# Kernel tuning notes

Hardware: AMD Instinct MI355X
Metric: run time of the kernel (lower is better)

## Reference

```python
import jax, jax.numpy as jnp
import numpy as np

K = 1024          # num_embeddings
D = 64            # embedding_dim
COMMIT = 0.25
DIVERSITY = 0.1


def setup_inputs() -> dict:
    key = jax.random.key(0)
    k1, k2 = jax.random.split(key)
    inputs = jax.random.normal(k1, (64, D, 32, 32), dtype=jnp.float32)
    emb = jax.random.uniform(k2, (K, D), dtype=jnp.float32,
                             minval=-1.0 / K, maxval=1.0 / K)
    return {"inputs": inputs, "emb": emb}


def reference(inputs, emb):
    # NCHW -> NHWC, flatten to [N, D]
    x = jnp.transpose(inputs, (0, 2, 3, 1))          # [B,H,W,D]
    flat = x.reshape(-1, D)                           # [N,D]

    dist = (jnp.sum(flat * flat, axis=1, keepdims=True)
            + jnp.sum(emb * emb, axis=1)
            - 2.0 * flat @ emb.T)
    idx = jnp.argmin(dist, axis=1)                    # [N]
    encodings = jax.nn.one_hot(idx, K, dtype=flat.dtype)  # [N,K]

    # codebook lookup (equivalent to encodings @ emb)
    quantized = jnp.take(emb, idx, axis=0).reshape(x.shape)  # [B,H,W,D]

    sg = jax.lax.stop_gradient
    e_latent_loss = jnp.mean((sg(quantized) - x) ** 2)
    q_latent_loss = jnp.mean((quantized - sg(x)) ** 2)

    avg_probs = jnp.mean(encodings, axis=0)           # [K]
    perplexity = jnp.exp(-jnp.sum(avg_probs * jnp.log(avg_probs + 1e-10)))
    diversity_loss = DIVERSITY * (K - perplexity) / K

    loss = q_latent_loss + COMMIT * e_latent_loss + diversity_loss

    # straight-through estimator
    quantized_st = x + sg(quantized - x)
    quant_out = jnp.transpose(quantized_st, (0, 3, 1, 2))  # NHWC -> NCHW

    return loss, quant_out, perplexity, encodings, idx[:, None]
```

## Files before the change

### kernel.cpp

```cpp
#include <hip/hip_runtime.h>
#include <math.h>

namespace {
constexpr int Kc = 1024;
constexpr int Dd = 64;

__device__ inline float np_sumsq64(const float* __restrict__ a) {
#pragma clang fp contract(off)
    float r[8];
    #pragma unroll
    for (int j = 0; j < 8; ++j) r[j] = a[j] * a[j];
    #pragma unroll
    for (int i = 8; i < 64; i += 8) {
        #pragma unroll
        for (int j = 0; j < 8; ++j) {
            float s = a[i + j] * a[i + j];
            r[j] = r[j] + s;
        }
    }
    return ((r[0] + r[1]) + (r[2] + r[3])) + ((r[4] + r[5]) + (r[6] + r[7]));
}

__global__ void k_ee(const float* __restrict__ emb, float* __restrict__ ee) {
    int k = blockIdx.x * blockDim.x + threadIdx.x;
    ee[k] = np_sumsq64(emb + (size_t)k * Dd);
}

__global__ __launch_bounds__(256, 4) void k_main(
    const float* __restrict__ inputs, const float* __restrict__ emb,
    const float* __restrict__ ee_g, float* __restrict__ quant,
    float* __restrict__ enc, float* __restrict__ idx_out,
    unsigned int* __restrict__ hist, float* __restrict__ partials)
{
    __shared__ float sb[4][64];
    __shared__ int   si[4][64];

    const int tid = threadIdx.x;
    const int p = __builtin_amdgcn_readfirstlane(tid >> 6);
    const int l = tid & 63;
    const int n = blockIdx.x * 64 + l;
    const int b = n >> 10;
    const int hw = n & 1023;

    const float* xin = inputs + (size_t)b * (Dd * 1024) + hw;
    float x[Dd];
    #pragma unroll
    for (int d = 0; d < Dd; ++d) x[d] = xin[d * 1024];

    const float xx = np_sumsq64(x);

    float4* enc4 = (float4*)enc + (size_t)blockIdx.x * 16384 + tid;

    float best = INFINITY;
    int i1 = 0;
    const int k0 = p * 256;
    for (int kk = 0; kk < 256; ++kk) {
        const int k = __builtin_amdgcn_readfirstlane(k0 + kk);
        const float* ek = emb + (size_t)k * Dd;
        float g = 0.f;
        #pragma unroll
        for (int d = 0; d < Dd; ++d) g = fmaf(x[d], ek[d], g);
        float A = xx + ee_g[k];
        float dist = fmaf(-2.f, g, A);
        bool lt = dist < best;
        best = lt ? dist : best;
        i1   = lt ? k    : i1;
        if ((kk & 3) == 0) {
            *enc4 = float4{0.f, 0.f, 0.f, 0.f};
            enc4 += 256;
        }
    }

    sb[p][l] = best; si[p][l] = i1;
    __syncthreads();

    if (tid < 64) {
        best = INFINITY; i1 = 0;
        #pragma unroll
        for (int q = 0; q < 4; ++q) {
            float s = sb[q][l];
            int   i = si[q][l];
            bool lt = s < best;
            best = lt ? s : best;
            i1   = lt ? i : i1;
        }

        {
            const float4* eb = (const float4*)(emb + (size_t)i1 * Dd);
            float* qout = quant + (size_t)b * (Dd * 1024) + hw;
            #pragma unroll
            for (int i = 0; i < Dd / 4; ++i) {
                float4 v = eb[i];
                qout[(i * 4 + 0) * 1024] = v.x;
                qout[(i * 4 + 1) * 1024] = v.y;
                qout[(i * 4 + 2) * 1024] = v.z;
                qout[(i * 4 + 3) * 1024] = v.w;
            }
        }

        idx_out[n] = (float)i1;
        atomicAdd(hist + i1, 1u);

        enc[(size_t)n * Kc + i1] = 1.0f;

        float v = best;
        #pragma unroll
        for (int off = 32; off > 0; off >>= 1) v += __shfl_down(v, off, 64);
        if (l == 0) partials[blockIdx.x] = v;
    }
}

__global__ __launch_bounds__(1024) void k_fin(
    const unsigned int* __restrict__ hist, const float* __restrict__ partials,
    float* __restrict__ loss_out, float* __restrict__ perp_out)
{
    __shared__ double sd[1024];
    int tid = threadIdx.x;
    double p = (double)hist[tid] * (1.0 / 65536.0);
    sd[tid] = p * log(p + 1e-10);
    __syncthreads();
    for (int s = 512; s > 0; s >>= 1) {
        if (tid < s) sd[tid] += sd[tid + s];
        __syncthreads();
    }
    double ent = sd[0];
    __syncthreads();
    sd[tid] = (double)partials[tid];
    __syncthreads();
    for (int s = 512; s > 0; s >>= 1) {
        if (tid < s) sd[tid] += sd[tid + s];
        __syncthreads();
    }
    if (tid == 0) {
        double perp = exp(-ent);
        double mean = sd[0] * (1.0 / 4194304.0);
        double loss = 1.25 * mean + 0.1 * (1024.0 - perp) / 1024.0;
        loss_out[0] = (float)loss;
        perp_out[0] = (float)perp;
    }
}
}

extern "C" void kernel_launch(void* const* d_in, const int* in_sizes, int n_in,
                              void* d_out, int out_size, void* d_ws, size_t ws_size,
                              hipStream_t stream)
{
    const float* inputs = (const float*)d_in[0];
    const float* emb    = (const float*)d_in[1];
    float* out = (float*)d_out;

    float* loss_out = out;
    float* quant    = out + 1;
    float* perp_out = out + 1 + 4194304;
    float* enc      = out + 2 + 4194304;
    float* idx_out  = out + 2 + 4194304 + 67108864;

    unsigned int* hist = (unsigned int*)d_ws;
    float* partials    = (float*)d_ws + 1024;
    float* ee          = (float*)d_ws + 2048;

    hipMemsetAsync(d_ws, 0, 2048 * sizeof(float), stream);
    k_ee<<<Kc / 256, 256, 0, stream>>>(emb, ee);
    k_main<<<65536 / 64, 256, 0, stream>>>(inputs, emb, ee, quant, enc, idx_out, hist, partials);
    k_fin<<<1, 1024, 0, stream>>>(hist, partials, loss_out, perp_out);
}
```

Measured before the change: 429.6 us.

## Unroll codebook scan by four, rotate start, fold memset, shuffle-reduce finalizer

The main distance loop now handles four codebook entries per iteration with independent accumulators. Each wave's starting point is rotated by block and wave index to spread L2 and scalar-cache pressure, and ties are broken by lowest index so results match the reference. The hist memset is folded into the ee kernel, and the finalizer reduction switches from a shared-memory tree to wave shuffles. The main intent is better ILP and fewer loop overheads, at the cost of more registers under the 256x4 launch bounds.

```diff
diff --git a/kernel.cpp b/kernel.cpp
--- a/kernel.cpp
+++ b/kernel.cpp
@@ -21,9 +21,11 @@
     return ((r[0] + r[1]) + (r[2] + r[3])) + ((r[4] + r[5]) + (r[6] + r[7]));
 }
 
-__global__ void k_ee(const float* __restrict__ emb, float* __restrict__ ee) {
+__global__ void k_ee(const float* __restrict__ emb, float* __restrict__ ee,
+                     unsigned int* __restrict__ hist) {
     int k = blockIdx.x * blockDim.x + threadIdx.x;
     ee[k] = np_sumsq64(emb + (size_t)k * Dd);
+    hist[k] = 0u;
 }
 
 __global__ __launch_bounds__(256, 4) void k_main(
@@ -54,33 +56,56 @@
     float best = INFINITY;
     int i1 = 0;
     const int k0 = p * 256;
-    for (int kk = 0; kk < 256; ++kk) {
-        const int k = __builtin_amdgcn_readfirstlane(k0 + kk);
-        const float* ek = emb + (size_t)k * Dd;
-        float g = 0.f;
+    const int rot = ((p + (int)blockIdx.x) & 3) * 16;
+
+    for (int qq = 0; qq < 64; ++qq) {
+        const int q = (qq + rot) & 63;
+        const int kb = __builtin_amdgcn_readfirstlane(k0 + q * 4);
+        const float* __restrict__ eb = emb + (size_t)kb * Dd;
+
+        float g0 = 0.f, g1 = 0.f, g2 = 0.f, g3 = 0.f;
         #pragma unroll
-        for (int d = 0; d < Dd; ++d) g = fmaf(x[d], ek[d], g);
-        float A = xx + ee_g[k];
-        float dist = fmaf(-2.f, g, A);
-        bool lt = dist < best;
-        best = lt ? dist : best;
-        i1   = lt ? k    : i1;
-        if ((kk & 3) == 0) {
-            *enc4 = float4{0.f, 0.f, 0.f, 0.f};
-            enc4 += 256;
+        for (int d = 0; d < Dd; ++d) {
+            const float xd = x[d];
+            g0 = fmaf(xd, eb[d],       g0);
+            g1 = fmaf(xd, eb[d + 64],  g1);
+            g2 = fmaf(xd, eb[d + 128], g2);
+            g3 = fmaf(xd, eb[d + 192], g3);
         }
+
+        const float A0 = xx + ee_g[kb];
+        const float A1 = xx + ee_g[kb + 1];
+        const float A2 = xx + ee_g[kb + 2];
+        const float A3 = xx + ee_g[kb + 3];
+        const float d0 = fmaf(-2.f, g0, A0);
+        const float d1 = fmaf(-2.f, g1, A1);
+        const float d2 = fmaf(-2.f, g2, A2);
+        const float d3 = fmaf(-2.f, g3, A3);
+
+        bool lt;
+        lt = (d0 < best) || (d0 == best && (kb + 0) < i1);
+        best = lt ? d0 : best;  i1 = lt ? kb + 0 : i1;
+        lt = (d1 < best) || (d1 == best && (kb + 1) < i1);
+        best = lt ? d1 : best;  i1 = lt ? kb + 1 : i1;
+        lt = (d2 < best) || (d2 == best && (kb + 2) < i1);
+        best = lt ? d2 : best;  i1 = lt ? kb + 2 : i1;
+        lt = (d3 < best) || (d3 == best && (kb + 3) < i1);
+        best = lt ? d3 : best;  i1 = lt ? kb + 3 : i1;
+
+        *enc4 = float4{0.f, 0.f, 0.f, 0.f};
+        enc4 += 256;
     }
 
     sb[p][l] = best; si[p][l] = i1;
     __syncthreads();
 
     if (tid < 64) {
-        best = INFINITY; i1 = 0;
+        best = INFINITY; i1 = 0x7fffffff;
         #pragma unroll
         for (int q = 0; q < 4; ++q) {
             float s = sb[q][l];
             int   i = si[q][l];
-            bool lt = s < best;
+            bool lt = (s < best) || (s == best && i < i1);
             best = lt ? s : best;
             i1   = lt ? i : i1;
         }
@@ -114,26 +139,28 @@
     const unsigned int* __restrict__ hist, const float* __restrict__ partials,
     float* __restrict__ loss_out, float* __restrict__ perp_out)
 {
-    __shared__ double sd[1024];
-    int tid = threadIdx.x;
-    double p = (double)hist[tid] * (1.0 / 65536.0);
-    sd[tid] = p * log(p + 1e-10);
+    __shared__ double sent[16];
+    __shared__ double spar[16];
+    const int tid = threadIdx.x;
+
+    double pv = (double)hist[tid] * (1.0 / 65536.0);
+    double e = pv * log(pv + 1e-10);
+    double s = (double)partials[tid];
+
+    #pragma unroll
+    for (int off = 32; off > 0; off >>= 1) {
+        e += __shfl_down(e, off, 64);
+        s += __shfl_down(s, off, 64);
+    }
+    if ((tid & 63) == 0) { sent[tid >> 6] = e; spar[tid >> 6] = s; }
     __syncthreads();
-    for (int s = 512; s > 0; s >>= 1) {
-        if (tid < s) sd[tid] += sd[tid + s];
-        __syncthreads();
-    }
-    double ent = sd[0];
-    __syncthreads();
-    sd[tid] = (double)partials[tid];
-    __syncthreads();
-    for (int s = 512; s > 0; s >>= 1) {
-        if (tid < s) sd[tid] += sd[tid + s];
-        __syncthreads();
-    }
+
     if (tid == 0) {
+        double ent = 0.0, sum = 0.0;
+        #pragma unroll
+        for (int w = 0; w < 16; ++w) { ent += sent[w]; sum += spar[w]; }
         double perp = exp(-ent);
-        double mean = sd[0] * (1.0 / 4194304.0);
+        double mean = sum * (1.0 / 4194304.0);
         double loss = 1.25 * mean + 0.1 * (1024.0 - perp) / 1024.0;
         loss_out[0] = (float)loss;
         perp_out[0] = (float)perp;
@@ -159,8 +186,7 @@
     float* partials    = (float*)d_ws + 1024;
     float* ee          = (float*)d_ws + 2048;
 
-    hipMemsetAsync(d_ws, 0, 2048 * sizeof(float), stream);
-    k_ee<<<Kc / 256, 256, 0, stream>>>(emb, ee);
+    k_ee<<<Kc / 256, 256, 0, stream>>>(emb, ee, hist);
     k_main<<<65536 / 64, 256, 0, stream>>>(inputs, emb, ee, quant, enc, idx_out, hist, partials);
     k_fin<<<1, 1024, 0, stream>>>(hist, partials, loss_out, perp_out);
 }
```

After: 512.5 us. 19.3% more time.
